# Performance work log

Hardware: AMD Instinct MI355X
Metric: run time of the kernel (lower is better)

The kernel has to match this reference:

```python
import jax, jax.numpy as jnp
import numpy as np

B = 1 << 20
BG_RANK = 16
H, W = 512, 1024  # bg_resolution * (H_mul=1, W_mul=2)
FEATC = 128


def equirect_unwrap(dirs):
    # dirs: [B,3] unit vectors -> grid coords in [-1,1], (gx indexes W, gy indexes H)
    phi = jnp.arctan2(dirs[:, 1], dirs[:, 0])            # [-pi, pi]
    theta = jnp.arccos(jnp.clip(dirs[:, 2], -1.0, 1.0))  # [0, pi]
    gx = phi / jnp.pi
    gy = theta / jnp.pi * 2.0 - 1.0
    return gx, gy


def grid_sample_bilinear(img, gx, gy):
    # img: [C,H,W]; gx,gy: [N]; align_corners=False, zero padding (torch default)
    C, Hh, Ww = img.shape
    ix = (gx + 1.0) * 0.5 * Ww - 0.5
    iy = (gy + 1.0) * 0.5 * Hh - 0.5
    x0 = jnp.floor(ix)
    y0 = jnp.floor(iy)
    x1 = x0 + 1.0
    y1 = y0 + 1.0
    wx1 = ix - x0
    wx0 = 1.0 - wx1
    wy1 = iy - y0
    wy0 = 1.0 - wy1

    def gather(xf, yf):
        valid = (xf >= 0) & (xf <= Ww - 1) & (yf >= 0) & (yf <= Hh - 1)
        xc = jnp.clip(xf, 0, Ww - 1).astype(jnp.int32)
        yc = jnp.clip(yf, 0, Hh - 1).astype(jnp.int32)
        v = img[:, yc, xc]  # [C, N]
        return v * valid.astype(img.dtype)

    out = (gather(x0, y0) * (wx0 * wy0)
           + gather(x1, y0) * (wx1 * wy0)
           + gather(x0, y1) * (wx0 * wy1)
           + gather(x1, y1) * (wx1 * wy1))
    return out  # [C, N]


def setup_inputs() -> dict:
    key = jax.random.key(0)
    k1, k2, k3, k4, k5 = jax.random.split(key, 5)
    viewdirs = jax.random.normal(k1, (B, 3), dtype=jnp.float32)
    viewdirs = viewdirs / jnp.linalg.norm(viewdirs, axis=-1, keepdims=True)
    roughness = jax.random.uniform(k2, (B,), dtype=jnp.float32)
    bg_mat = 0.1 * jax.random.normal(k3, (BG_RANK, H, W), dtype=jnp.float32)
    # bias-free Linear weights, stored [in, out]
    W1 = jax.random.normal(k4, (BG_RANK, FEATC), dtype=jnp.float32) / np.sqrt(BG_RANK)
    W2 = jax.random.normal(k5, (FEATC, 3), dtype=jnp.float32) / np.sqrt(FEATC)
    return {"viewdirs": viewdirs, "roughness": roughness,
            "bg_mat": bg_mat, "W1": W1, "W2": W2}


def reference(viewdirs, roughness, bg_mat, W1, W2):
    gx, gy = equirect_unwrap(viewdirs)
    emb = grid_sample_bilinear(bg_mat, gx, gy).T  # [B, bg_rank]
    h = jax.nn.relu(emb @ W1)                     # [B, featureC]
    return jax.nn.softplus(h @ W2)                # [B, 3]
```

## Files before the change

kernel.cpp:

```cpp
#include <hip/hip_runtime.h>
#include <hip/hip_fp16.h>
#include <math.h>

#define NB    (1 << 20)
#define HH    512
#define WW    1024
#define RANK  16
#define FC    128
#define HW    (HH * WW)
#define TPB   256

#define FP8_SCALE  64.0f
#define FP8_ISCALE 0.015625f

typedef float        f32x16 __attribute__((ext_vector_type(16)));
typedef float        f32x2  __attribute__((ext_vector_type(2)));
typedef _Float16     f16x8  __attribute__((ext_vector_type(8)));
typedef _Float16     h2     __attribute__((ext_vector_type(2)));
typedef unsigned int uint2v __attribute__((ext_vector_type(2)));

__device__ __forceinline__ h2 pkrtz(float a, float b) {
    return __builtin_bit_cast(h2, __builtin_amdgcn_cvt_pkrtz(a, b));
}
__device__ __forceinline__ h2 relu2(h2 a) {
    h2 r;
    r[0] = (a[0] > (_Float16)0.0f) ? a[0] : (_Float16)0.0f;
    r[1] = (a[1] > (_Float16)0.0f) ? a[1] : (_Float16)0.0f;
    return r;
}

__device__ __forceinline__ float fast_atan2f(float y, float x) {
    float ax = fabsf(x), ay = fabsf(y);
    float mx = fmaxf(ax, ay), mn = fminf(ax, ay);
    float z  = __fdividef(mn, mx);
    if (mx == 0.0f) z = 0.0f;
    bool  red = z > 0.41421356f;
    float zr  = red ? __fdividef(z - 1.0f, z + 1.0f) : z;
    float t2  = zr * zr;
    float p   = (((0.0805374449f * t2 - 0.138776856f) * t2
                 + 0.199777106f) * t2 - 0.333329491f) * t2 * zr + zr;
    if (red)      p += 0.78539816339f;
    if (ay > ax)  p  = 1.57079632679f - p;
    if (x < 0.0f) p  = 3.14159265359f - p;
    return copysignf(p, y);
}
__device__ __forceinline__ float fast_acosf(float x) {
    float xa = fabsf(x);
    float p = -0.0012624911f;
    p = p * xa + 0.0066700901f;
    p = p * xa - 0.0170881256f;
    p = p * xa + 0.0308918810f;
    p = p * xa - 0.0501743046f;
    p = p * xa + 0.0889789874f;
    p = p * xa - 0.2145988016f;
    p = p * xa + 1.5707963050f;
    float r = sqrtf(1.0f - xa) * p;
    return x >= 0.0f ? r : 3.14159265359f - r;
}
__device__ __forceinline__ float softplusf(float a) {
    return fmaxf(a, 0.0f) + __logf(1.0f + __expf(-fabsf(a)));
}

__global__ __launch_bounds__(256) void prep_kernel(
    const float* __restrict__ bg,
    const float* __restrict__ W1,
    const float* __restrict__ W2,
    uint4* __restrict__ tex8,
    f16x8* __restrict__ table)
{
    const int base = (blockIdx.x * 256 + threadIdx.x) * 2;
    float2 v[RANK];
    #pragma unroll
    for (int c = 0; c < RANK; ++c)
        v[c] = *(const float2*)(bg + (size_t)c * HW + base);

    #pragma unroll
    for (int j = 0; j < 2; ++j) {
        float c[RANK];
        #pragma unroll
        for (int ch = 0; ch < RANK; ++ch)
            c[ch] = (j ? v[ch].y : v[ch].x) * FP8_SCALE;
        union { unsigned u[4]; uint4 q; } o;
        #pragma unroll
        for (int d = 0; d < 4; ++d) {
            int w = __builtin_amdgcn_cvt_pk_fp8_f32(c[4*d + 0], c[4*d + 1], 0, false);
            w     = __builtin_amdgcn_cvt_pk_fp8_f32(c[4*d + 2], c[4*d + 3], w, true);
            o.u[d] = (unsigned)w;
        }
        tex8[base + j] = o.q;
    }

    if (blockIdx.x == 0 && threadIdx.x < 64) {
        const int lane = threadIdx.x;
        const int l31  = lane & 31;
        const int q5   = (lane >> 5) & 1;
        #pragma unroll
        for (int jt = 0; jt < 4; ++jt) {
            f16x8 w;
            #pragma unroll
            for (int ii = 0; ii < 8; ++ii)
                w[ii] = (_Float16)W1[(8 * q5 + ii) * FC + 32 * jt + l31];
            table[jt * 64 + lane] = w;
        }
        const bool ok = ((l31 & 3) < 3) && (l31 < 8);
        const int  c3 = l31 & 3;
        #pragma unroll
        for (int kt = 0; kt < 8; ++kt) {
            f16x8 w;
            #pragma unroll
            for (int ii = 0; ii < 8; ++ii) {
                const int n = 16 * kt + 8 * (ii >> 2) + 4 * q5 + (ii & 3);
                w[ii] = ok ? (_Float16)W2[3 * n + c3] : (_Float16)0.0f;
            }
            table[(4 + kt) * 64 + lane] = w;
        }
    }
}

template <int MODE>
__global__ __launch_bounds__(TPB, 4) void bg_render_mfma(
    const float* __restrict__ viewdirs,
    const void*  __restrict__ srcv,
    const f16x8* __restrict__ ftab,
    const float* __restrict__ W1,
    const float* __restrict__ W2,
    float* __restrict__ out)
{
    const int tid  = threadIdx.x;
    const int lane = tid & 63;
    const int l31  = tid & 31;
    const int q5   = (tid >> 5) & 1;

    const f32x16 kZero = {0.f,0.f,0.f,0.f,0.f,0.f,0.f,0.f,
                          0.f,0.f,0.f,0.f,0.f,0.f,0.f,0.f};

    const int i = blockIdx.x * TPB + tid;

    const float dx = viewdirs[3 * i + 0];
    const float dy = viewdirs[3 * i + 1];
    const float dz = viewdirs[3 * i + 2];
    const float INV_PI = 0.31830988618379067154f;
    float phi   = fast_atan2f(dy, dx);
    float theta = fast_acosf(fminf(fmaxf(dz, -1.0f), 1.0f));
    float gx = phi * INV_PI;
    float gy = theta * (2.0f * INV_PI) - 1.0f;

    float ix = (gx + 1.0f) * (0.5f * (float)WW) - 0.5f;
    float iy = (gy + 1.0f) * (0.5f * (float)HH) - 0.5f;
    float x0f = floorf(ix), y0f = floorf(iy);
    float wx1 = ix - x0f, wx0 = 1.0f - wx1;
    float wy1 = iy - y0f, wy0 = 1.0f - wy1;
    int x0 = (int)x0f, y0 = (int)y0f;
    int x1 = x0 + 1,   y1 = y0 + 1;

    float w00 = wx0 * wy0, w10 = wx1 * wy0, w01 = wx0 * wy1, w11 = wx1 * wy1;
    bool vx0 = (x0 >= 0) & (x0 <= WW - 1);
    bool vx1 = (x1 >= 0) & (x1 <= WW - 1);
    bool vy0 = (y0 >= 0) & (y0 <= HH - 1);
    bool vy1 = (y1 >= 0) & (y1 <= HH - 1);
    if (!(vx0 & vy0)) w00 = 0.0f;
    if (!(vx1 & vy0)) w10 = 0.0f;
    if (!(vx0 & vy1)) w01 = 0.0f;
    if (!(vx1 & vy1)) w11 = 0.0f;

    int cx0 = min(max(x0, 0), WW - 1), cx1 = min(max(x1, 0), WW - 1);
    int cy0 = min(max(y0, 0), HH - 1), cy1 = min(max(y1, 0), HH - 1);
    int b00 = cy0 * WW + cx0, b10 = cy0 * WW + cx1;
    int b01 = cy1 * WW + cx0, b11 = cy1 * WW + cx1;

    h2 e[8];
    f16x8 w1f[4], w2f[8];
    if (MODE == 0) {
        const uint4* tex = (const uint4*)srcv;
        uint4 t00 = tex[b00];
        uint4 t10 = tex[b10];
        uint4 t01 = tex[b01];
        uint4 t11 = tex[b11];

        #pragma unroll
        for (int f = 0; f < 4; ++f) w1f[f] = ftab[f * 64 + lane];
        #pragma unroll
        for (int f = 0; f < 8; ++f) w2f[f] = ftab[(4 + f) * 64 + lane];

        float ef[RANK];
        #pragma unroll
        for (int ch = 0; ch < RANK; ++ch) ef[ch] = 0.0f;
        const float s00 = w00 * FP8_ISCALE, s10 = w10 * FP8_ISCALE;
        const float s01 = w01 * FP8_ISCALE, s11 = w11 * FP8_ISCALE;

        auto acc_tap = [&](const uint4& t, float w) {
            const unsigned u[4] = {t.x, t.y, t.z, t.w};
            #pragma unroll
            for (int d = 0; d < 4; ++d) {
                f32x2 lo = __builtin_amdgcn_cvt_pk_f32_fp8((int)u[d], false);
                f32x2 hi = __builtin_amdgcn_cvt_pk_f32_fp8((int)u[d], true);
                ef[4*d + 0] = fmaf(lo.x, w, ef[4*d + 0]);
                ef[4*d + 1] = fmaf(lo.y, w, ef[4*d + 1]);
                ef[4*d + 2] = fmaf(hi.x, w, ef[4*d + 2]);
                ef[4*d + 3] = fmaf(hi.y, w, ef[4*d + 3]);
            }
        };
        acc_tap(t00, s00);
        acc_tap(t10, s10);
        acc_tap(t01, s01);
        acc_tap(t11, s11);

        #pragma unroll
        for (int d = 0; d < 8; ++d)
            e[d] = pkrtz(ef[2 * d], ef[2 * d + 1]);
    } else {
        const float* src = (const float*)srcv;
        float ef[RANK];
        #pragma unroll
        for (int ch = 0; ch < RANK; ++ch) {
            const float* img = src + ch * HW;
            ef[ch] = img[b00] * w00 + img[b10] * w10
                   + img[b01] * w01 + img[b11] * w11;
        }
        #pragma unroll
        for (int d = 0; d < 8; ++d)
            e[d] = pkrtz(ef[2 * d], ef[2 * d + 1]);

        #pragma unroll
        for (int jt = 0; jt < 4; ++jt) {
            f16x8 v;
            #pragma unroll
            for (int ii = 0; ii < 8; ++ii)
                v[ii] = (_Float16)W1[(8 * q5 + ii) * FC + 32 * jt + l31];
            w1f[jt] = v;
        }
        const bool ok = ((l31 & 3) < 3) && (l31 < 8);
        const int  c3 = l31 & 3;
        #pragma unroll
        for (int kt = 0; kt < 8; ++kt) {
            f16x8 v;
            #pragma unroll
            for (int ii = 0; ii < 8; ++ii) {
                const int n = 16 * kt + 8 * (ii >> 2) + 4 * q5 + (ii & 3);
                v[ii] = ok ? (_Float16)W2[3 * n + c3] : (_Float16)0.0f;
            }
            w2f[kt] = v;
        }
    }

    union FragU { f16x8 v; h2 h[4]; unsigned int u[4]; };
    FragU bq0, bq1;
    #pragma unroll
    for (int d = 0; d < 4; ++d) {
        unsigned int lo = __builtin_bit_cast(unsigned int, e[d]);
        unsigned int hi = __builtin_bit_cast(unsigned int, e[d + 4]);
        uint2v r = __builtin_amdgcn_permlane32_swap(lo, hi, false, false);
        bq0.u[d] = r.x;
        bq1.u[d] = r.y;
    }

    float ag[2][3];
    #pragma unroll
    for (int g = 0; g < 2; ++g) {
        const f16x8 bq = (g == 0) ? bq0.v : bq1.v;
        f32x16 acc = kZero;
        #pragma unroll
        for (int jt = 0; jt < 4; ++jt) {
            f32x16 h = __builtin_amdgcn_mfma_f32_32x32x16_f16(w1f[jt], bq, kZero, 0, 0, 0);
            FragU plo, phi_;
            #pragma unroll
            for (int r = 0; r < 4; ++r) {
                plo.h[r]  = relu2(pkrtz(h[2*r],     h[2*r + 1]));
                phi_.h[r] = relu2(pkrtz(h[8 + 2*r], h[8 + 2*r + 1]));
            }
            acc = __builtin_amdgcn_mfma_f32_32x32x16_f16(w2f[2*jt],     plo.v,  acc, 0, 0, 0);
            acc = __builtin_amdgcn_mfma_f32_32x32x16_f16(w2f[2*jt + 1], phi_.v, acc, 0, 0, 0);
        }
        ag[g][0] = acc[0]; ag[g][1] = acc[1]; ag[g][2] = acc[2];
    }

    float a0 = q5 ? ag[1][0] : ag[0][0];
    float a1 = q5 ? ag[1][1] : ag[0][1];
    float a2 = q5 ? ag[1][2] : ag[0][2];

    out[3 * i + 0] = softplusf(a0);
    out[3 * i + 1] = softplusf(a1);
    out[3 * i + 2] = softplusf(a2);
}

extern "C" void kernel_launch(void* const* d_in, const int* in_sizes, int n_in,
                              void* d_out, int out_size, void* d_ws, size_t ws_size,
                              hipStream_t stream) {
    const float* viewdirs = (const float*)d_in[0];
    const float* bg_mat   = (const float*)d_in[2];
    const float* W1       = (const float*)d_in[3];
    const float* W2       = (const float*)d_in[4];
    float* out            = (float*)d_out;

    const size_t tex_bytes = (size_t)HW * 16;
    const size_t tab_bytes = (size_t)12 * 64 * sizeof(f16x8);
    const int nblocks = NB / TPB;

    if (ws_size >= tex_bytes + tab_bytes) {
        uint4*  tex8 = (uint4*)d_ws;
        f16x8*  ftab = (f16x8*)((char*)d_ws + tex_bytes);
        prep_kernel<<<dim3(HW / 512), dim3(256), 0, stream>>>(bg_mat, W1, W2, tex8, ftab);
        bg_render_mfma<0><<<dim3(nblocks), dim3(TPB), 0, stream>>>(
            viewdirs, (const void*)tex8, ftab, W1, W2, out);
    } else {
        bg_render_mfma<1><<<dim3(nblocks), dim3(TPB), 0, stream>>>(
            viewdirs, (const void*)bg_mat, nullptr, W1, W2, out);
    }
}
```

Before: 48.47 us.

## Store 2x2 bilinear neighbourhood per texel so each sample reads one contiguous 64-byte block

```diff
diff --git a/kernel.cpp b/kernel.cpp
--- a/kernel.cpp
+++ b/kernel.cpp
@@ -61,6 +61,79 @@
     return fmaxf(a, 0.0f) + __logf(1.0f + __expf(-fabsf(a)));
 }
 
+__device__ __forceinline__ void build_table(
+    const float* __restrict__ W1, const float* __restrict__ W2,
+    f16x8* __restrict__ table, int lane)
+{
+    const int l31 = lane & 31;
+    const int q5  = (lane >> 5) & 1;
+    #pragma unroll
+    for (int jt = 0; jt < 4; ++jt) {
+        f16x8 w;
+        #pragma unroll
+        for (int ii = 0; ii < 8; ++ii)
+            w[ii] = (_Float16)W1[(8 * q5 + ii) * FC + 32 * jt + l31];
+        table[jt * 64 + lane] = w;
+    }
+    const bool ok = ((l31 & 3) < 3) && (l31 < 8);
+    const int  c3 = l31 & 3;
+    #pragma unroll
+    for (int kt = 0; kt < 8; ++kt) {
+        f16x8 w;
+        #pragma unroll
+        for (int ii = 0; ii < 8; ++ii) {
+            const int n = 16 * kt + 8 * (ii >> 2) + 4 * q5 + (ii & 3);
+            w[ii] = ok ? (_Float16)W2[3 * n + c3] : (_Float16)0.0f;
+        }
+        table[(4 + kt) * 64 + lane] = w;
+    }
+}
+
+__global__ __launch_bounds__(256) void prep_quad_kernel(
+    const float* __restrict__ bg,
+    const float* __restrict__ W1,
+    const float* __restrict__ W2,
+    uint4* __restrict__ texq,
+    f16x8* __restrict__ table)
+{
+    const int e  = blockIdx.x * 256 + threadIdx.x;
+    const int x  = e & (WW - 1);
+    const int y  = e >> 10;
+    const int xp = min(x + 1, WW - 1);
+    const int yn = min(y + 1, HH - 1);
+    const int r0 = y * WW, r1 = yn * WW;
+
+    float v[4][RANK];
+    #pragma unroll
+    for (int c = 0; c < RANK; ++c) {
+        const float* img = bg + (size_t)c * HW;
+        v[0][c] = img[r0 + x];
+        v[1][c] = img[r0 + xp];
+        v[2][c] = img[r1 + x];
+        v[3][c] = img[r1 + xp];
+    }
+
+    uint4 o[4];
+    #pragma unroll
+    for (int s = 0; s < 4; ++s) {
+        union { unsigned u[4]; uint4 q; } pk;
+        #pragma unroll
+        for (int d = 0; d < 4; ++d) {
+            int w = __builtin_amdgcn_cvt_pk_fp8_f32(
+                        v[s][4*d + 0] * FP8_SCALE, v[s][4*d + 1] * FP8_SCALE, 0, false);
+            w     = __builtin_amdgcn_cvt_pk_fp8_f32(
+                        v[s][4*d + 2] * FP8_SCALE, v[s][4*d + 3] * FP8_SCALE, w, true);
+            pk.u[d] = (unsigned)w;
+        }
+        o[s] = pk.q;
+    }
+    uint4* dst = texq + 4 * (size_t)e;
+    dst[0] = o[0]; dst[1] = o[1]; dst[2] = o[2]; dst[3] = o[3];
+
+    if (blockIdx.x == 0 && threadIdx.x < 64)
+        build_table(W1, W2, table, threadIdx.x);
+}
+
 __global__ __launch_bounds__(256) void prep_kernel(
     const float* __restrict__ bg,
     const float* __restrict__ W1,
@@ -89,32 +162,8 @@
         }
         tex8[base + j] = o.q;
     }
-
-    if (blockIdx.x == 0 && threadIdx.x < 64) {
-        const int lane = threadIdx.x;
-        const int l31  = lane & 31;
-        const int q5   = (lane >> 5) & 1;
-        #pragma unroll
-        for (int jt = 0; jt < 4; ++jt) {
-            f16x8 w;
-            #pragma unroll
-            for (int ii = 0; ii < 8; ++ii)
-                w[ii] = (_Float16)W1[(8 * q5 + ii) * FC + 32 * jt + l31];
-            table[jt * 64 + lane] = w;
-        }
-        const bool ok = ((l31 & 3) < 3) && (l31 < 8);
-        const int  c3 = l31 & 3;
-        #pragma unroll
-        for (int kt = 0; kt < 8; ++kt) {
-            f16x8 w;
-            #pragma unroll
-            for (int ii = 0; ii < 8; ++ii) {
-                const int n = 16 * kt + 8 * (ii >> 2) + 4 * q5 + (ii & 3);
-                w[ii] = ok ? (_Float16)W2[3 * n + c3] : (_Float16)0.0f;
-            }
-            table[(4 + kt) * 64 + lane] = w;
-        }
-    }
+    if (blockIdx.x == 0 && threadIdx.x < 64)
+        build_table(W1, W2, table, threadIdx.x);
 }
 
 template <int MODE>
@@ -165,28 +214,33 @@
 
     int cx0 = min(max(x0, 0), WW - 1), cx1 = min(max(x1, 0), WW - 1);
     int cy0 = min(max(y0, 0), HH - 1), cy1 = min(max(y1, 0), HH - 1);
-    int b00 = cy0 * WW + cx0, b10 = cy0 * WW + cx1;
-    int b01 = cy1 * WW + cx0, b11 = cy1 * WW + cx1;
 
     h2 e[8];
     f16x8 w1f[4], w2f[8];
+
     if (MODE == 0) {
-        const uint4* tex = (const uint4*)srcv;
-        uint4 t00 = tex[b00];
-        uint4 t10 = tex[b10];
-        uint4 t01 = tex[b01];
-        uint4 t11 = tex[b11];
+        const int xb = min(max(x0, 0), WW - 2);
+        const int yb = min(max(y0, 0), HH - 2);
+        const uint4* p = (const uint4*)srcv + 4 * (size_t)(yb * WW + xb);
+        uint4 t0 = p[0], t1 = p[1], t2 = p[2], t3 = p[3];
 
         #pragma unroll
         for (int f = 0; f < 4; ++f) w1f[f] = ftab[f * 64 + lane];
         #pragma unroll
         for (int f = 0; f < 8; ++f) w2f[f] = ftab[(4 + f) * 64 + lane];
 
+        const int i0 = cx0 - xb, i1 = cx1 - xb;
+        const int j0 = cy0 - yb, j1 = cy1 - yb;
+        const int t00s = j0 * 2 + i0, t10s = j0 * 2 + i1;
+        const int t01s = j1 * 2 + i0, t11s = j1 * 2 + i1;
+        float s0 = (t00s==0?w00:0.f)+(t10s==0?w10:0.f)+(t01s==0?w01:0.f)+(t11s==0?w11:0.f);
+        float s1 = (t00s==1?w00:0.f)+(t10s==1?w10:0.f)+(t01s==1?w01:0.f)+(t11s==1?w11:0.f);
+        float s2 = (t00s==2?w00:0.f)+(t10s==2?w10:0.f)+(t01s==2?w01:0.f)+(t11s==2?w11:0.f);
+        float s3 = (t00s==3?w00:0.f)+(t10s==3?w10:0.f)+(t01s==3?w01:0.f)+(t11s==3?w11:0.f);
+
         float ef[RANK];
         #pragma unroll
         for (int ch = 0; ch < RANK; ++ch) ef[ch] = 0.0f;
-        const float s00 = w00 * FP8_ISCALE, s10 = w10 * FP8_ISCALE;
-        const float s01 = w01 * FP8_ISCALE, s11 = w11 * FP8_ISCALE;
 
         auto acc_tap = [&](const uint4& t, float w) {
             const unsigned u[4] = {t.x, t.y, t.z, t.w};
@@ -200,15 +254,54 @@
                 ef[4*d + 3] = fmaf(hi.y, w, ef[4*d + 3]);
             }
         };
-        acc_tap(t00, s00);
-        acc_tap(t10, s10);
-        acc_tap(t01, s01);
-        acc_tap(t11, s11);
+        acc_tap(t0, s0 * FP8_ISCALE);
+        acc_tap(t1, s1 * FP8_ISCALE);
+        acc_tap(t2, s2 * FP8_ISCALE);
+        acc_tap(t3, s3 * FP8_ISCALE);
+
+        #pragma unroll
+        for (int d = 0; d < 8; ++d)
+            e[d] = pkrtz(ef[2 * d], ef[2 * d + 1]);
+    } else if (MODE == 2) {
+        const int b00 = cy0 * WW + cx0, b10 = cy0 * WW + cx1;
+        const int b01 = cy1 * WW + cx0, b11 = cy1 * WW + cx1;
+        const uint4* tex = (const uint4*)srcv;
+        uint4 t00 = tex[b00];
+        uint4 t10 = tex[b10];
+        uint4 t01 = tex[b01];
+        uint4 t11 = tex[b11];
+
+        #pragma unroll
+        for (int f = 0; f < 4; ++f) w1f[f] = ftab[f * 64 + lane];
+        #pragma unroll
+        for (int f = 0; f < 8; ++f) w2f[f] = ftab[(4 + f) * 64 + lane];
+
+        float ef[RANK];
+        #pragma unroll
+        for (int ch = 0; ch < RANK; ++ch) ef[ch] = 0.0f;
+        auto acc_tap = [&](const uint4& t, float w) {
+            const unsigned u[4] = {t.x, t.y, t.z, t.w};
+            #pragma unroll
+            for (int d = 0; d < 4; ++d) {
+                f32x2 lo = __builtin_amdgcn_cvt_pk_f32_fp8((int)u[d], false);
+                f32x2 hi = __builtin_amdgcn_cvt_pk_f32_fp8((int)u[d], true);
+                ef[4*d + 0] = fmaf(lo.x, w, ef[4*d + 0]);
+                ef[4*d + 1] = fmaf(lo.y, w, ef[4*d + 1]);
+                ef[4*d + 2] = fmaf(hi.x, w, ef[4*d + 2]);
+                ef[4*d + 3] = fmaf(hi.y, w, ef[4*d + 3]);
+            }
+        };
+        acc_tap(t00, w00 * FP8_ISCALE);
+        acc_tap(t10, w10 * FP8_ISCALE);
+        acc_tap(t01, w01 * FP8_ISCALE);
+        acc_tap(t11, w11 * FP8_ISCALE);
 
         #pragma unroll
         for (int d = 0; d < 8; ++d)
             e[d] = pkrtz(ef[2 * d], ef[2 * d + 1]);
     } else {
+        const int b00 = cy0 * WW + cx0, b10 = cy0 * WW + cx1;
+        const int b01 = cy1 * WW + cx0, b11 = cy1 * WW + cx1;
         const float* src = (const float*)srcv;
         float ef[RANK];
         #pragma unroll
@@ -292,15 +385,22 @@
     const float* W2       = (const float*)d_in[4];
     float* out            = (float*)d_out;
 
-    const size_t tex_bytes = (size_t)HW * 16;
-    const size_t tab_bytes = (size_t)12 * 64 * sizeof(f16x8);
+    const size_t quad_bytes = (size_t)HW * 64;
+    const size_t t16_bytes  = (size_t)HW * 16;
+    const size_t tab_bytes  = (size_t)12 * 64 * sizeof(f16x8);
     const int nblocks = NB / TPB;
 
-    if (ws_size >= tex_bytes + tab_bytes) {
+    if (ws_size >= quad_bytes + tab_bytes) {
+        uint4*  texq = (uint4*)d_ws;
+        f16x8*  ftab = (f16x8*)((char*)d_ws + quad_bytes);
+        prep_quad_kernel<<<dim3(HW / 256), dim3(256), 0, stream>>>(bg_mat, W1, W2, texq, ftab);
+        bg_render_mfma<0><<<dim3(nblocks), dim3(TPB), 0, stream>>>(
+            viewdirs, (const void*)texq, ftab, W1, W2, out);
+    } else if (ws_size >= t16_bytes + tab_bytes) {
         uint4*  tex8 = (uint4*)d_ws;
-        f16x8*  ftab = (f16x8*)((char*)d_ws + tex_bytes);
+        f16x8*  ftab = (f16x8*)((char*)d_ws + t16_bytes);
         prep_kernel<<<dim3(HW / 512), dim3(256), 0, stream>>>(bg_mat, W1, W2, tex8, ftab);
-        bg_render_mfma<0><<<dim3(nblocks), dim3(TPB), 0, stream>>>(
+        bg_render_mfma<2><<<dim3(nblocks), dim3(TPB), 0, stream>>>(
             viewdirs, (const void*)tex8, ftab, W1, W2, out);
     } else {
         bg_render_mfma<1><<<dim3(nblocks), dim3(TPB), 0, stream>>>(
```

Result: slower. 54.01 us (+11.4%).
